# Optimization experiments

Hardware: AMD Instinct MI355X
Metric: run time of the kernel (lower is better)

## Reference

```python
import jax, jax.numpy as jnp
import numpy as np

# Dims: T=out_seq_len, B=batch, D=hidden_dim, H=hidden_dim_de, E=embedding_size, C=feat_channels
T, B, D, H, E, C, FH, FW = 32, 16, 512, 512, 512, 512, 8, 32


def _lstm_dir(x_seq, W_ih, W_hh, b_ih, b_hh, reverse):
    # x_seq: (T, B, D); PyTorch gate order i, f, g, o
    gx = jnp.einsum('tbd,gd->tbg', x_seq, W_ih) + b_ih  # (T, B, 4H)
    Hh = W_hh.shape[1]
    def step(carry, g_t):
        h, c = carry
        g = g_t + h @ W_hh.T + b_hh
        i, f, gg, o = jnp.split(g, 4, axis=-1)
        c = jax.nn.sigmoid(f) * c + jax.nn.sigmoid(i) * jnp.tanh(gg)
        h = jax.nn.sigmoid(o) * jnp.tanh(c)
        return (h, c), h
    init = (jnp.zeros((x_seq.shape[1], Hh), x_seq.dtype),
            jnp.zeros((x_seq.shape[1], Hh), x_seq.dtype))
    _, hs = jax.lax.scan(step, init, gx, reverse=reverse)
    return hs  # (T, B, H)


def setup_inputs() -> dict:
    key = jax.random.key(0)
    ks = jax.random.split(key, 16)
    s = 0.02
    inp = {
        'hidden_en': jax.random.normal(ks[0], (T, B, D), jnp.float32),
        'conv_f': jax.random.normal(ks[1], (B, C, FH, FW), jnp.float32),
        # bidirectional LSTM params (PyTorch layout: W_ih (4H, D), W_hh (4H, H))
        'W_ih_f': jax.random.normal(ks[2], (4 * H, D), jnp.float32) * s,
        'W_hh_f': jax.random.normal(ks[3], (4 * H, H), jnp.float32) * s,
        'b_ih_f': jnp.zeros((4 * H,), jnp.float32),
        'b_hh_f': jnp.zeros((4 * H,), jnp.float32),
        'W_ih_b': jax.random.normal(ks[4], (4 * H, D), jnp.float32) * s,
        'W_hh_b': jax.random.normal(ks[5], (4 * H, H), jnp.float32) * s,
        'b_ih_b': jnp.zeros((4 * H,), jnp.float32),
        'b_hh_b': jnp.zeros((4 * H,), jnp.float32),
        # linear_decode: (H, 2H)
        'W_dec': jax.random.normal(ks[6], (H, 2 * H), jnp.float32) * s,
        'b_dec': jnp.zeros((H,), jnp.float32),
        # conv_em: 3x3, C -> E (OIHW)
        'W_em': jax.random.normal(ks[7], (E, C, 3, 3), jnp.float32) * s,
        'b_em': jnp.zeros((E,), jnp.float32),
        # attention h_em: 1x1 conv == linear H -> E
        'W_hem': jax.random.normal(ks[8], (E, H), jnp.float32) * s,
        'b_hem': jnp.zeros((E,), jnp.float32),
        # conv_att: 1x1 conv E -> 1
        'w_att': jax.random.normal(ks[9], (E,), jnp.float32) * s,
        'b_att': jnp.zeros((), jnp.float32),
    }
    return inp


def reference(hidden_en, conv_f, W_ih_f, W_hh_f, b_ih_f, b_hh_f,
              W_ih_b, W_hh_b, b_ih_b, b_hh_b, W_dec, b_dec,
              W_em, b_em, W_hem, b_hem, w_att, b_att):
    # decoder_ctc: bidirectional LSTM + linear
    h_fwd = _lstm_dir(hidden_en, W_ih_f, W_hh_f, b_ih_f, b_hh_f, reverse=False)
    h_bwd = _lstm_dir(hidden_en, W_ih_b, W_hh_b, b_ih_b, b_hh_b, reverse=True)
    hidden_de = jnp.concatenate([h_fwd, h_bwd], axis=-1) @ W_dec.T + b_dec  # (T, B, H)

    # conv_em: 3x3 same-padding conv, NCHW
    x_em = jax.lax.conv_general_dilated(
        conv_f, W_em, window_strides=(1, 1), padding='SAME',
        dimension_numbers=('NCHW', 'OIHW', 'NCHW')) + b_em[None, :, None, None]  # (B,E,FH,FW)
    att_x_em = jnp.transpose(x_em.reshape(x_em.shape[0], E, -1), (0, 2, 1))  # (B, HW, E)

    # batched attention over all timesteps (dropout is identity at eval)
    h_em = jnp.einsum('tbh,eh->tbe', hidden_de, W_hem) + b_hem  # (T, B, E)
    feat = jnp.tanh(x_em[None] + h_em[:, :, :, None, None])     # (T, B, E, FH, FW)
    scores = jnp.einsum('tbehw,e->tbhw', feat, w_att) + b_att   # (T, B, FH, FW)
    alpha = jax.nn.softmax(scores.reshape(scores.shape[0], scores.shape[1], -1), axis=-1)  # (T,B,HW)
    att = jnp.einsum('tbn,bne->tbe', alpha, att_x_em)           # (T, B, E)

    ctc_out = jnp.concatenate([hidden_de, att], axis=-1)        # (T, B, H+E)
    return jnp.transpose(ctc_out, (1, 0, 2))                    # (B, T, H+E)
```

## Files before the change

### kernel.cpp

```cpp
#include <hip/hip_runtime.h>
#include <hip/hip_bf16.h>
#include <math.h>

#define T_LEN 32
#define BATCH 16
#define DDIM  512
#define HDIM  512
#define EDIM  512
#define CDIM  512
#define FHH   8
#define FWW   32
#define HW    256
#define G4    2048
#define PADH  10
#define PADW  34
#define WLP   520

typedef __attribute__((ext_vector_type(8))) short bf16x8;
typedef __attribute__((ext_vector_type(4))) float f32x4;

__device__ __forceinline__ ushort bfr(float x) {
    union { float f; uint32_t u; } c; c.f = x;
    uint32_t r = (c.u + 0x7FFFu + ((c.u >> 16) & 1u)) >> 16;
    return (ushort)r;
}

__device__ __forceinline__ float frcp(float x) { return __builtin_amdgcn_rcpf(x); }
__device__ __forceinline__ float ftanh(float x) {
    return 1.f - 2.f * frcp(1.f + __expf(2.f * x));
}
__device__ __forceinline__ float fsig(float x) {
    return frcp(1.f + __expf(-x));
}

__device__ __forceinline__ void ld_lds16(const void* g, void* l) {
    __builtin_amdgcn_global_load_lds((const __attribute__((address_space(1))) void*)g,
                                     (__attribute__((address_space(3))) void*)l, 16, 0, 0);
}

__device__ __forceinline__ void st_u16_sc1(ushort* p, ushort v) {
    asm volatile("global_store_short %0, %1, off sc1" :: "v"(p), "v"((uint)v) : "memory");
}
__device__ __forceinline__ void st_i32_sc1(int* p, int v) {
    asm volatile("global_store_dword %0, %1, off sc1" :: "v"(p), "v"(v) : "memory");
}
__device__ __forceinline__ void st_f32_sc1(float* p, float v) {
    asm volatile("global_store_dword %0, %1, off sc1" :: "v"(p), "v"(v) : "memory");
}
__device__ __forceinline__ int ld_i32_sc1(const int* p) {
    int v;
    asm volatile("global_load_dword %0, %1, off sc1\n\ts_waitcnt vmcnt(0)"
                 : "=v"(v) : "v"(p) : "memory");
    return v;
}
__device__ __forceinline__ float ld_f32_sc1(const float* p) {
    float v;
    asm volatile("global_load_dword %0, %1, off sc1\n\ts_waitcnt vmcnt(0)"
                 : "=v"(v) : "v"(p) : "memory");
    return v;
}

struct PrepArgs { const float* s[7]; ushort* d[7]; };
__global__ __launch_bounds__(256) void prep_all(
    PrepArgs a, int* __restrict__ syncbuf,
    const float* __restrict__ conv_f, ushort* __restrict__ padT,
    const float* __restrict__ W_em, ushort* __restrict__ Wt,
    const float* __restrict__ W_dec, ushort* __restrict__ WdecT,
    const float* __restrict__ W_hem, const float* __restrict__ b_dec,
    const float* __restrict__ b_hem, float* __restrict__ b_comb)
{
    __shared__ float tile[32][33];
    const int bid = blockIdx.x, tid = threadIdx.x;
    if (bid < 5120) {
        int i = bid * 256 + tid;
        if (i < 80) st_i32_sc1(syncbuf + i, 0);
        const int e0 = 65536, e1 = 327680, e2 = 589824, e3 = 851968,
                  e4 = 1114112, e5 = 1245184;
        int seg, base;
        if      (i < e0) { seg = 0; base = 0;  }
        else if (i < e1) { seg = 1; base = e0; }
        else if (i < e2) { seg = 2; base = e1; }
        else if (i < e3) { seg = 3; base = e2; }
        else if (i < e4) { seg = 4; base = e3; }
        else if (i < e5) { seg = 5; base = e4; }
        else             { seg = 6; base = e5; }
        int li = i - base;
        float4 v = ((const float4*)a.s[seg])[li];
        ushort4 o;
        o.x = bfr(v.x); o.y = bfr(v.y); o.z = bfr(v.z); o.w = bfr(v.w);
        ((ushort4*)a.d[seg])[li] = o;
        return;
    }
    if (bid < 7168) {
        int id = bid - 5120;
        int s0 = (id & 7) * 32, c0 = ((id >> 3) & 15) * 32, b = id >> 7;
        int lo = tid & 31, hi = tid >> 5;
#pragma unroll
        for (int it = 0; it < 4; ++it) {
            int cl = hi + it * 8;
            tile[cl][lo] = conv_f[((size_t)(b * CDIM + c0 + cl)) * HW + s0 + lo];
        }
        __syncthreads();
#pragma unroll
        for (int it = 0; it < 4; ++it) {
            int sl = hi + it * 8;
            int s = s0 + sl;
            int y = s >> 5, x = s & 31;
            padT[(((size_t)b * PADH + y + 1) * PADW + (x + 1)) * CDIM + c0 + lo] =
                bfr(tile[lo][sl]);
        }
        return;
    }
    if (bid < 7840) {
        int gid = (bid - 7168) * 256 + tid;
        int c4 = gid & 127;
        int cellb = gid >> 7;
        int cell = cellb % 84;
        int b = cellb / 84;
        int y, x;
        if (cell < 34) { y = 0; x = cell; }
        else if (cell < 68) { y = 9; x = cell - 34; }
        else { int k2 = cell - 68; y = 1 + (k2 >> 1); x = (k2 & 1) ? 33 : 0; }
        ((ushort4*)padT)[(((size_t)b * PADH + y) * PADW + x) * (CDIM / 4) + c4] =
            make_ushort4(0, 0, 0, 0);
        return;
    }
    if (bid < 17056) {
        int gid = (bid - 7840) * 256 + tid;
        int c = gid % CDIM;
        int t = gid / CDIM;
        int e = t % EDIM;
        int tap = t / EDIM;
        int dy = tap / 3, dx = tap % 3;
        Wt[gid] = bfr(W_em[((e * CDIM + c) * 3 + dy) * 3 + dx]);
        return;
    }
    if (bid < 17568) {
        int idx = bid - 17056;
        int ht = idx & 15, kt = idx >> 4;
        int h0 = ht * 32, k0 = kt * 32;
        int lo = tid & 31, hi = tid >> 5;
#pragma unroll
        for (int it = 0; it < 4; ++it) {
            int i = hi + it * 8;
            tile[i][lo] = W_dec[(size_t)(h0 + i) * 1024 + k0 + lo];
        }
        __syncthreads();
#pragma unroll
        for (int it = 0; it < 4; ++it) {
            int i = hi + it * 8;
            WdecT[(size_t)(k0 + i) * 512 + h0 + lo] = bfr(tile[lo][i]);
        }
        return;
    }
    {
        int e = (bid - 17568) * 256 + tid;
        float s = b_hem[e];
        const float* wr = W_hem + (size_t)e * 512;
        for (int h = 0; h < 512; ++h) s += wr[h] * b_dec[h];
        b_comb[e] = s;
    }
}

__device__ __forceinline__ void tile64_compute(
    const ushort* Ap0, const ushort* Bp0, int K,
    ushort* smem, int tid, f32x4 (&acc)[2][2])
{
    ushort* As = smem;
    ushort* Bs = smem + 2048;
    const int w = tid >> 6, lane = tid & 63;
    ushort* AsW = &As[w * 512];
    ushort* BsW = &Bs[w * 512];
    const int wm = (w >> 1) * 32, wn = (w & 1) * 32;
    const int kb = (lane >> 4) * 8, fr = lane & 15;
    for (int kk = 0; kk < K; kk += 32) {
        __syncthreads();
        ld_lds16(Ap0 + kk, AsW);
        ld_lds16(Bp0 + kk, BsW);
        __syncthreads();
        bf16x8 af[2], bg[2];
#pragma unroll
        for (int i = 0; i < 2; ++i)
            af[i] = *(const bf16x8*)&As[(wm + i * 16 + fr) * 32 + kb];
#pragma unroll
        for (int j = 0; j < 2; ++j)
            bg[j] = *(const bf16x8*)&Bs[(wn + j * 16 + fr) * 32 + kb];
#pragma unroll
        for (int i = 0; i < 2; ++i)
#pragma unroll
            for (int j = 0; j < 2; ++j)
                acc[i][j] = __builtin_amdgcn_mfma_f32_16x16x32_bf16(af[i], bg[j], acc[i][j], 0, 0, 0);
    }
}

__global__ __launch_bounds__(256) void workers(
    const ushort* __restrict__ padT, const ushort* __restrict__ Wt,
    const float* __restrict__ bias_em, float* __restrict__ xem,
    const ushort* __restrict__ hen_bf,
    const ushort* __restrict__ Wih_f, const ushort* __restrict__ Wih_b,
    const float* __restrict__ b_ih_f, const float* __restrict__ b_hh_f,
    const float* __restrict__ b_ih_b, const float* __restrict__ b_hh_b,
    float* __restrict__ gxT_f, float* __restrict__ gxT_b,
    const ushort* __restrict__ Whem_bf, const ushort* __restrict__ WdecT_bf,
    ushort* __restrict__ Wcomb_bf)
{
    __shared__ ushort smem[4096];
    const int bid = blockIdx.x, tid = threadIdx.x;
    const int w = tid >> 6, lane = tid & 63;
    const int r0 = tid >> 2, c0 = (tid & 3) * 8;
    const int wm = (w >> 1) * 32, wn = (w & 1) * 32;
    const int col = lane & 15, rq = (lane >> 4) * 4;
    f32x4 acc[2][2];
#pragma unroll
    for (int i = 0; i < 2; ++i)
#pragma unroll
        for (int j = 0; j < 2; ++j) acc[i][j] = {0.f, 0.f, 0.f, 0.f};

    if (bid < 512) {
        const int n0 = (bid & 7) * 64, m0 = (bid >> 3) * 64;
        const int b = m0 >> 8, s0 = m0 & 255, y0 = s0 >> 5;
        const int y = y0 + (r0 >> 5), x = r0 & 31;
        const ushort* Abase = padT + (((size_t)b * PADH + y) * PADW + x) * CDIM + c0;
        const ushort* Bbase = Wt + (size_t)(n0 + r0) * CDIM + c0;
        for (int tap = 0; tap < 9; ++tap) {
            const int dy = tap / 3, dx = tap % 3;
            tile64_compute(Abase + ((size_t)dy * PADW + dx) * CDIM,
                           Bbase + (size_t)tap * EDIM * CDIM, 512, smem, tid, acc);
        }
#pragma unroll
        for (int i = 0; i < 2; ++i)
#pragma unroll
            for (int r = 0; r < 4; ++r) {
                int m = m0 + wm + i * 16 + rq + r;
                int s = m & 255;
#pragma unroll
                for (int j2 = 0; j2 < 2; ++j2) {
                    int e = n0 + wn + j2 * 16 + col;
                    xem[((size_t)b * EDIM + e) * HW + s] = acc[i][j2][r] + bias_em[e];
                }
            }
        return;
    }
    if (bid < 1024) {
        const int gi = bid - 512;
        const int dir = gi & 1;
        const int q = gi >> 1;
        const int mt = q >> 5, nt = q & 31;
        const ushort* Bw = dir ? Wih_b : Wih_f;
        const float* bi0 = dir ? b_ih_b : b_ih_f;
        const float* bi1 = dir ? b_hh_b : b_hh_f;
        float* Cg = dir ? gxT_b : gxT_f;
        const int m0 = mt * 64, n0 = nt * 64;
        tile64_compute(hen_bf + (size_t)(m0 + r0) * 512 + c0,
                       Bw + (size_t)(n0 + r0) * 512 + c0, 512, smem, tid, acc);
#pragma unroll
        for (int i = 0; i < 2; ++i)
#pragma unroll
            for (int r = 0; r < 4; ++r) {
                int m = m0 + wm + i * 16 + rq + r;
#pragma unroll
                for (int j2 = 0; j2 < 2; ++j2) {
                    int n = n0 + wn + j2 * 16 + col;
                    Cg[(size_t)m * G4 + (n & 511) * 4 + (n >> 9)] =
                        acc[i][j2][r] + bi0[n] + bi1[n];
                }
            }
        return;
    }
    {
        const int wb = bid - 1024;
        const int mt = wb >> 4, nt = wb & 15;
        const int m0 = mt * 64, n0 = nt * 64;
        tile64_compute(Whem_bf + (size_t)(m0 + r0) * 512 + c0,
                       WdecT_bf + (size_t)(n0 + r0) * 512 + c0, 512, smem, tid, acc);
#pragma unroll
        for (int i = 0; i < 2; ++i)
#pragma unroll
            for (int r = 0; r < 4; ++r) {
                int m = m0 + wm + i * 16 + rq + r;
#pragma unroll
                for (int j2 = 0; j2 < 2; ++j2) {
                    int n = n0 + wn + j2 * 16 + col;
                    Wcomb_bf[(size_t)m * 1024 + n] = bfr(acc[i][j2][r]);
                }
            }
    }
}

__global__ __launch_bounds__(256) void lstm_persist(
    const ushort* __restrict__ Whh_f, const ushort* __restrict__ Whh_b,
    const float* __restrict__ gxT_f, const float* __restrict__ gxT_b,
    ushort* __restrict__ hs_bf, int* __restrict__ flags)
{
    __shared__ ushort smem[64 * WLP];
    const int bid = blockIdx.x, tid = threadIdx.x;
    const int w = tid >> 6, lane = tid & 63;
    const int dir = bid >> 5;
    const int j0 = (bid & 31) * 16;
    const ushort* W = dir ? Whh_b : Whh_f;
    const float* gx = dir ? gxT_b : gxT_f;
#pragma unroll
    for (int i = 0; i < 16; ++i) {
        int row = w * 16 + i;
        int g = row >> 4, jl = row & 15;
        bf16x8 v = *(const bf16x8*)(W + ((size_t)(g * 512 + j0 + jl)) * 512 + lane * 8);
        *(bf16x8*)&smem[row * WLP + lane * 8] = v;
    }
    __syncthreads();
    if (tid >= 64) return;
    __builtin_amdgcn_s_setprio(1);

    const int fr = lane & 15, kq = lane >> 4;
    const int j = j0 + fr;
    const int* fq = &flags[dir * 32 + (lane & 31)];
    f32x4 cr = {0.f, 0.f, 0.f, 0.f};
    for (int step = 0; step < T_LEN; ++step) {
        const int tcur = dir ? (T_LEN - 1 - step) : step;
        float4 gq[4];
#pragma unroll
        for (int r = 0; r < 4; ++r)
            gq[r] = *(const float4*)(gx + (((size_t)tcur * BATCH + kq * 4 + r) * 512 + j) * 4);
        f32x4 acc[4];
#pragma unroll
        for (int g = 0; g < 4; ++g) acc[g] = {0.f, 0.f, 0.f, 0.f};
        if (step > 0) {
            const int tprev = dir ? tcur + 1 : tcur - 1;
            const ushort* hp = hs_bf + ((size_t)tprev * BATCH + fr) * 1024 + dir * 512 + kq * 8;
            bf16x8 hreg[16];
#pragma unroll
            for (int u = 0; u < 16; ++u)
                asm volatile("global_load_dwordx4 %0, %1, off sc1"
                             : "=v"(hreg[u]) : "v"(hp + u * 32));
            asm volatile("s_waitcnt vmcnt(0)" ::: "memory");
            __builtin_amdgcn_sched_barrier(0);
#pragma unroll
            for (int u = 0; u < 16; ++u) {
#pragma unroll
                for (int g = 0; g < 4; ++g) {
                    bf16x8 bb = *(const bf16x8*)&smem[(g * 16 + fr) * WLP + kq * 8 + u * 32];
                    acc[g] = __builtin_amdgcn_mfma_f32_16x16x32_bf16(hreg[u], bb, acc[g], 0, 0, 0);
                }
            }
        }
#pragma unroll
        for (int r = 0; r < 4; ++r) {
            int b = kq * 4 + r;
            float gi = gq[r].x + acc[0][r];
            float gf = gq[r].y + acc[1][r];
            float gg = gq[r].z + acc[2][r];
            float go = gq[r].w + acc[3][r];
            float si = fsig(gi), sf = fsig(gf), so = fsig(go);
            float c = sf * cr[r] + si * ftanh(gg);
            cr[r] = c;
            float h = so * ftanh(c);
            st_u16_sc1(hs_bf + ((size_t)tcur * BATCH + b) * 1024 + dir * 512 + j, bfr(h));
        }
        if (step < T_LEN - 1) {
            asm volatile("s_waitcnt vmcnt(0)" ::: "memory");
            if (lane == 0) st_i32_sc1(&flags[bid], step + 1);
            const int need = step + 1;
            for (;;) {
                int v = ld_i32_sc1(fq);
                if (__all(v >= need)) break;
                __builtin_amdgcn_s_sleep(1);
            }
        }
    }
}

__global__ __launch_bounds__(256) void tail(
    const ushort* __restrict__ hs_bf, const ushort* __restrict__ Wdec_bf,
    const float* __restrict__ b_dec, float* __restrict__ out,
    const ushort* __restrict__ Wcomb_bf, const float* __restrict__ b_comb,
    float* __restrict__ h_em,
    const float* __restrict__ xem, const float* __restrict__ watt,
    int* __restrict__ syncbuf)
{
    __shared__ ushort smem[4096];
    int* hcnt = syncbuf + 64;
    const int bid = blockIdx.x, tid = threadIdx.x;
    const int w = tid >> 6, lane = tid & 63;
    const int r0 = tid >> 2, c0 = (tid & 3) * 8;
    const int wm = (w >> 1) * 32, wn = (w & 1) * 32;
    const int col = lane & 15, rq = (lane >> 4) * 4;

    if (bid < 128) {
        f32x4 acc[2][2];
#pragma unroll
        for (int i = 0; i < 2; ++i)
#pragma unroll
            for (int j = 0; j < 2; ++j) acc[i][j] = {0.f, 0.f, 0.f, 0.f};
        if (bid < 64) {
            const int mt = bid >> 3, nt = bid & 7;
            const int m0 = mt * 64, n0 = nt * 64;
            tile64_compute(hs_bf + (size_t)(m0 + r0) * 1024 + c0,
                           Wdec_bf + (size_t)(n0 + r0) * 1024 + c0, 1024, smem, tid, acc);
#pragma unroll
            for (int i = 0; i < 2; ++i)
#pragma unroll
                for (int r = 0; r < 4; ++r) {
                    int m = m0 + wm + i * 16 + rq + r;
                    int t = m >> 4, b = m & 15;
#pragma unroll
                    for (int j2 = 0; j2 < 2; ++j2) {
                        int n = n0 + wn + j2 * 16 + col;
                        out[((size_t)(b * T_LEN + t)) * 1024 + n] = acc[i][j2][r] + b_dec[n];
                    }
                }
        } else {
            const int blk = bid - 64;
            const int mt = blk >> 3, nt = blk & 7;
            const int m0 = mt * 64, n0 = nt * 64;
            tile64_compute(hs_bf + (size_t)(m0 + r0) * 1024 + c0,
                           Wcomb_bf + (size_t)(n0 + r0) * 1024 + c0, 1024, smem, tid, acc);
#pragma unroll
            for (int i = 0; i < 2; ++i)
#pragma unroll
                for (int r = 0; r < 4; ++r) {
                    int m = m0 + wm + i * 16 + rq + r;
#pragma unroll
                    for (int j2 = 0; j2 < 2; ++j2) {
                        int n = n0 + wn + j2 * 16 + col;
                        st_f32_sc1(&h_em[(size_t)m * 512 + n], acc[i][j2][r] + b_comb[n]);
                    }
                }
            asm volatile("s_waitcnt vmcnt(0)" ::: "memory");
            __syncthreads();
            if (tid == 0) atomicAdd(&hcnt[mt], 1);
        }
        return;
    }

    {
        int i = bid - 128;
        int k = i >> 3;
        int b = ((i & 7) << 1) | (k & 1);
        int t = k >> 1;
        int tb = t * 16 + b;
        const int mt = tb >> 6;
        if (tid == 0) {
            while (ld_i32_sc1(&hcnt[mt]) < 8) __builtin_amdgcn_s_sleep(8);
        }
        __syncthreads();
        float* fs = (float*)smem;
        float* hl = fs;
        float* wl = fs + 512;
        float* al = fs + 1024;
        float* red = fs + 1280;
        for (int q = tid; q < 512; q += 256) {
            hl[q] = ld_f32_sc1(&h_em[(size_t)tb * 512 + q]);
            wl[q] = watt[q];
        }
        __syncthreads();
        const float* xb = xem + (size_t)b * EDIM * HW;
        float sc = 0.f;
#pragma unroll 4
        for (int e = 0; e < 512; ++e)
            sc += ftanh(xb[(size_t)e * HW + tid] + hl[e]) * wl[e];
        float m = sc;
#pragma unroll
        for (int o = 32; o; o >>= 1) m = fmaxf(m, __shfl_xor(m, o));
        if ((tid & 63) == 0) red[tid >> 6] = m;
        __syncthreads();
        m = fmaxf(fmaxf(red[0], red[1]), fmaxf(red[2], red[3]));
        float ex = __expf(sc - m);
        float s = ex;
#pragma unroll
        for (int o = 32; o; o >>= 1) s += __shfl_xor(s, o);
        if ((tid & 63) == 0) red[4 + (tid >> 6)] = s;
        __syncthreads();
        s = red[4] + red[5] + red[6] + red[7];
        al[tid] = ex * frcp(s);
        __syncthreads();
        float* ob = out + ((size_t)(b * T_LEN + t)) * 1024 + 512;
        for (int eo = 0; eo < 512; eo += 256) {
            int e = eo + tid;
            const float* xr = xb + (size_t)e * HW;
            float acc2 = 0.f;
#pragma unroll 4
            for (int n = 0; n < 256; n += 4) {
                float4 v = *(const float4*)&xr[n];
                acc2 += al[n] * v.x + al[n + 1] * v.y + al[n + 2] * v.z + al[n + 3] * v.w;
            }
            ob[e] = acc2;
        }
    }
}

extern "C" void kernel_launch(void* const* d_in, const int* in_sizes, int n_in,
                              void* d_out, int out_size, void* d_ws, size_t ws_size,
                              hipStream_t stream) {
    const float* hidden_en = (const float*)d_in[0];
    const float* conv_f    = (const float*)d_in[1];
    const float* W_ih_f    = (const float*)d_in[2];
    const float* W_hh_f    = (const float*)d_in[3];
    const float* b_ih_f    = (const float*)d_in[4];
    const float* b_hh_f    = (const float*)d_in[5];
    const float* W_ih_b    = (const float*)d_in[6];
    const float* W_hh_b    = (const float*)d_in[7];
    const float* b_ih_b    = (const float*)d_in[8];
    const float* b_hh_b    = (const float*)d_in[9];
    const float* W_dec     = (const float*)d_in[10];
    const float* b_dec     = (const float*)d_in[11];
    const float* W_em      = (const float*)d_in[12];
    const float* b_em      = (const float*)d_in[13];
    const float* W_hem     = (const float*)d_in[14];
    const float* b_hem     = (const float*)d_in[15];
    const float* w_att     = (const float*)d_in[16];
    float* out = (float*)d_out;

    char* p = (char*)d_ws;
    auto alloc = [&](size_t bytes) { void* r = p; p += (bytes + 255) & ~(size_t)255; return r; };
    float*    gxT_f   = (float*)alloc((size_t)T_LEN * BATCH * G4 * 4);
    float*    gxT_b   = (float*)alloc((size_t)T_LEN * BATCH * G4 * 4);
    float*    h_em    = (float*)alloc((size_t)T_LEN * BATCH * 512 * 4);
    float*    x_em    = (float*)alloc((size_t)BATCH * EDIM * HW * 4);
    ushort*   padT    = (ushort*)alloc((size_t)BATCH * PADH * PADW * CDIM * 2);
    ushort*   Wt      = (ushort*)alloc((size_t)9 * EDIM * CDIM * 2);
    ushort*   hen_bf  = (ushort*)alloc((size_t)T_LEN * BATCH * DDIM * 2);
    ushort*   Wihf_bf = (ushort*)alloc((size_t)G4 * DDIM * 2);
    ushort*   Wihb_bf = (ushort*)alloc((size_t)G4 * DDIM * 2);
    ushort*   Whhf_bf = (ushort*)alloc((size_t)G4 * HDIM * 2);
    ushort*   Whhb_bf = (ushort*)alloc((size_t)G4 * HDIM * 2);
    ushort*   Wdec_bf = (ushort*)alloc((size_t)HDIM * 1024 * 2);
    ushort*   Whem_bf = (ushort*)alloc((size_t)EDIM * HDIM * 2);
    ushort*   WdecT_bf= (ushort*)alloc((size_t)1024 * 512 * 2);
    ushort*   Wcomb_bf= (ushort*)alloc((size_t)512 * 1024 * 2);
    float*    b_comb  = (float*)alloc(512 * 4);
    ushort*   hs_bf   = (ushort*)alloc((size_t)T_LEN * BATCH * 1024 * 2);
    int*      syncbuf = (int*)alloc(512);

    PrepArgs pa;
    pa.s[0] = hidden_en; pa.d[0] = hen_bf;
    pa.s[1] = W_ih_f;    pa.d[1] = Wihf_bf;
    pa.s[2] = W_ih_b;    pa.d[2] = Wihb_bf;
    pa.s[3] = W_hh_f;    pa.d[3] = Whhf_bf;
    pa.s[4] = W_hh_b;    pa.d[4] = Whhb_bf;
    pa.s[5] = W_dec;     pa.d[5] = Wdec_bf;
    pa.s[6] = W_hem;     pa.d[6] = Whem_bf;
    prep_all<<<17570, 256, 0, stream>>>(pa, syncbuf, conv_f, padT, W_em, Wt,
                                        W_dec, WdecT_bf, W_hem, b_dec, b_hem, b_comb);

    workers<<<1152, 256, 0, stream>>>(padT, Wt, b_em, x_em, hen_bf,
                                      Wihf_bf, Wihb_bf, b_ih_f, b_hh_f,
                                      b_ih_b, b_hh_b, gxT_f, gxT_b,
                                      Whem_bf, WdecT_bf, Wcomb_bf);

    lstm_persist<<<64, 256, 0, stream>>>(Whhf_bf, Whhb_bf, gxT_f, gxT_b,
                                         hs_bf, syncbuf);

    tail<<<640, 256, 0, stream>>>(hs_bf, Wdec_bf, b_dec, out,
                                  Wcomb_bf, b_comb, h_em, x_em, w_att, syncbuf);
}
```

Baseline: 287.4 us.

## Fuse LSTM recurrence into worker kernel with per-timestep-tile readiness counters

The persistent LSTM recurrence now runs as the first 64 blocks of a merged kernel that also holds the input-projection GEMM, the conv GEMM and the weight-combine GEMM. Input-projection tiles are ordered by timestep, with the backward direction reversed, and each completed tile bumps a counter so the recurrence can start as soon as the timesteps it needs are ready. This is meant to overlap the serial recurrence with the conv and other GEMM work instead of running them back to back. The gate-preactivation load for the next step is also prefetched asynchronously, and the flag poll reads four flags per vector load. The risk is that the 64 recurrence blocks, each using about 96KB of LDS, must be resident alongside the spin-waiting producers, and conv blocks may compete with the recurrence for compute.

After: 280.2 us. -2.5%, faster.

```diff
diff --git a/kernel.cpp b/kernel.cpp
--- a/kernel.cpp
+++ b/kernel.cpp
@@ -18,6 +18,7 @@
 
 typedef __attribute__((ext_vector_type(8))) short bf16x8;
 typedef __attribute__((ext_vector_type(4))) float f32x4;
+typedef __attribute__((ext_vector_type(4))) int i32x4;
 
 __device__ __forceinline__ ushort bfr(float x) {
     union { float f; uint32_t u; } c; c.f = x;
@@ -53,10 +54,21 @@
                  : "=v"(v) : "v"(p) : "memory");
     return v;
 }
+__device__ __forceinline__ i32x4 ld_i32x4_sc1(const int* p) {
+    i32x4 v;
+    asm volatile("global_load_dwordx4 %0, %1, off sc1\n\ts_waitcnt vmcnt(0)"
+                 : "=v"(v) : "v"(p) : "memory");
+    return v;
+}
 __device__ __forceinline__ float ld_f32_sc1(const float* p) {
     float v;
     asm volatile("global_load_dword %0, %1, off sc1\n\ts_waitcnt vmcnt(0)"
                  : "=v"(v) : "v"(p) : "memory");
+    return v;
+}
+__device__ __forceinline__ f32x4 ld_f32x4_sc1_async(const float* p) {
+    f32x4 v;
+    asm volatile("global_load_dwordx4 %0, %1, off sc1" : "=v"(v) : "v"(p));
     return v;
 }
 
@@ -73,7 +85,7 @@
     const int bid = blockIdx.x, tid = threadIdx.x;
     if (bid < 5120) {
         int i = bid * 256 + tid;
-        if (i < 80) st_i32_sc1(syncbuf + i, 0);
+        if (i < 128) st_i32_sc1(syncbuf + i, 0);
         const int e0 = 65536, e1 = 327680, e2 = 589824, e3 = 851968,
                   e4 = 1114112, e5 = 1245184;
         int seg, base;
@@ -193,20 +205,123 @@
     }
 }
 
-__global__ __launch_bounds__(256) void workers(
-    const ushort* __restrict__ padT, const ushort* __restrict__ Wt,
-    const float* __restrict__ bias_em, float* __restrict__ xem,
+__global__ __launch_bounds__(256) void fused_main(
+    const ushort* __restrict__ Whh_f, const ushort* __restrict__ Whh_b,
+    float* __restrict__ gxT_f, float* __restrict__ gxT_b,
     const ushort* __restrict__ hen_bf,
     const ushort* __restrict__ Wih_f, const ushort* __restrict__ Wih_b,
     const float* __restrict__ b_ih_f, const float* __restrict__ b_hh_f,
     const float* __restrict__ b_ih_b, const float* __restrict__ b_hh_b,
-    float* __restrict__ gxT_f, float* __restrict__ gxT_b,
+    ushort* __restrict__ hs_bf,
+    int* __restrict__ syncbuf,
+    const ushort* __restrict__ padT, const ushort* __restrict__ Wt,
+    const float* __restrict__ bias_em, float* __restrict__ xem,
     const ushort* __restrict__ Whem_bf, const ushort* __restrict__ WdecT_bf,
     ushort* __restrict__ Wcomb_bf)
 {
-    __shared__ ushort smem[4096];
+    __shared__ ushort smem[49152];
     const int bid = blockIdx.x, tid = threadIdx.x;
     const int w = tid >> 6, lane = tid & 63;
+    int* flags = syncbuf;
+    int* gcnt  = syncbuf + 64;
+
+    if (bid < 64) {
+        const int dir = bid >> 5;
+        const int j0 = (bid & 31) * 16;
+        const ushort* W = dir ? Whh_b : Whh_f;
+        const float* gx = dir ? gxT_b : gxT_f;
+#pragma unroll
+        for (int i = 0; i < 16; ++i) {
+            int row = w * 16 + i;
+            int g = row >> 4, jl = row & 15;
+            bf16x8 v = *(const bf16x8*)(W + ((size_t)(g * 512 + j0 + jl)) * 512 + lane * 8);
+            *(bf16x8*)&smem[row * WLP + lane * 8] = v;
+        }
+        __syncthreads();
+        if (tid >= 64) return;
+        __builtin_amdgcn_s_setprio(1);
+
+        const int fr = lane & 15, kq = lane >> 4;
+        const int j = j0 + fr;
+        const int* fq4 = &flags[dir * 32 + (lane & 7) * 4];
+        const int t0 = dir ? (T_LEN - 1) : 0;
+        int mt_ok = t0 >> 2;
+        {
+            const int* gp = &gcnt[dir * 8 + mt_ok];
+            while (ld_i32_sc1(gp) < 32) __builtin_amdgcn_s_sleep(4);
+        }
+        f32x4 gq[4];
+#pragma unroll
+        for (int r = 0; r < 4; ++r)
+            gq[r] = ld_f32x4_sc1_async(gx + (((size_t)t0 * BATCH + kq * 4 + r) * 512 + j) * 4);
+        f32x4 cr = {0.f, 0.f, 0.f, 0.f};
+        for (int step = 0; step < T_LEN; ++step) {
+            const int tcur = dir ? (T_LEN - 1 - step) : step;
+            if (step > 0) {
+                const int need = step;
+                for (;;) {
+                    i32x4 v = ld_i32x4_sc1(fq4);
+                    int mn = min(min(v[0], v[1]), min(v[2], v[3]));
+                    if (__all(mn >= need)) break;
+                    __builtin_amdgcn_s_sleep(1);
+                }
+            }
+            f32x4 acc[4];
+#pragma unroll
+            for (int g = 0; g < 4; ++g) acc[g] = {0.f, 0.f, 0.f, 0.f};
+            if (step > 0) {
+                const int tprev = dir ? tcur + 1 : tcur - 1;
+                const ushort* hp = hs_bf + ((size_t)tprev * BATCH + fr) * 1024 + dir * 512 + kq * 8;
+                bf16x8 hreg[16];
+#pragma unroll
+                for (int u = 0; u < 16; ++u)
+                    asm volatile("global_load_dwordx4 %0, %1, off sc1"
+                                 : "=v"(hreg[u]) : "v"(hp + u * 32));
+                asm volatile("s_waitcnt vmcnt(0)" ::: "memory");
+                __builtin_amdgcn_sched_barrier(0);
+#pragma unroll
+                for (int u = 0; u < 16; ++u) {
+#pragma unroll
+                    for (int g = 0; g < 4; ++g) {
+                        bf16x8 bb = *(const bf16x8*)&smem[(g * 16 + fr) * WLP + kq * 8 + u * 32];
+                        acc[g] = __builtin_amdgcn_mfma_f32_16x16x32_bf16(hreg[u], bb, acc[g], 0, 0, 0);
+                    }
+                }
+            } else {
+                asm volatile("s_waitcnt vmcnt(0)" ::: "memory");
+                __builtin_amdgcn_sched_barrier(0);
+            }
+#pragma unroll
+            for (int r = 0; r < 4; ++r) {
+                int b = kq * 4 + r;
+                float gi = gq[r][0] + acc[0][r];
+                float gf = gq[r][1] + acc[1][r];
+                float gg = gq[r][2] + acc[2][r];
+                float go = gq[r][3] + acc[3][r];
+                float si = fsig(gi), sf = fsig(gf), so = fsig(go);
+                float c = sf * cr[r] + si * ftanh(gg);
+                cr[r] = c;
+                float h = so * ftanh(c);
+                st_u16_sc1(hs_bf + ((size_t)tcur * BATCH + b) * 1024 + dir * 512 + j, bfr(h));
+            }
+            if (step < T_LEN - 1) {
+                asm volatile("s_waitcnt vmcnt(0)" ::: "memory");
+                if (lane == 0) st_i32_sc1(&flags[bid], step + 1);
+                const int tnext = dir ? tcur - 1 : tcur + 1;
+                const int mtn = tnext >> 2;
+                if (mtn != mt_ok) {
+                    const int* gp = &gcnt[dir * 8 + mtn];
+                    while (ld_i32_sc1(gp) < 32) __builtin_amdgcn_s_sleep(2);
+                    mt_ok = mtn;
+                }
+#pragma unroll
+                for (int r = 0; r < 4; ++r)
+                    gq[r] = ld_f32x4_sc1_async(gx + (((size_t)tnext * BATCH + kq * 4 + r) * 512 + j) * 4);
+            }
+        }
+        return;
+    }
+
     const int r0 = tid >> 2, c0 = (tid & 3) * 8;
     const int wm = (w >> 1) * 32, wn = (w & 1) * 32;
     const int col = lane & 15, rq = (lane >> 4) * 4;
@@ -216,8 +331,40 @@
 #pragma unroll
         for (int j = 0; j < 2; ++j) acc[i][j] = {0.f, 0.f, 0.f, 0.f};
 
-    if (bid < 512) {
-        const int n0 = (bid & 7) * 64, m0 = (bid >> 3) * 64;
+    if (bid < 576) {
+        const int gi = bid - 64;
+        const int dir = gi & 1;
+        const int q = gi >> 1;
+        const int nt = q & 31;
+        const int mt0 = q >> 5;
+        const int mtile = dir ? (7 - mt0) : mt0;
+        const ushort* Bw = dir ? Wih_b : Wih_f;
+        const float* bi0 = dir ? b_ih_b : b_ih_f;
+        const float* bi1 = dir ? b_hh_b : b_hh_f;
+        float* Cg = dir ? gxT_b : gxT_f;
+        const int m0 = mtile * 64, n0 = nt * 64;
+        tile64_compute(hen_bf + (size_t)(m0 + r0) * 512 + c0,
+                       Bw + (size_t)(n0 + r0) * 512 + c0, 512, smem, tid, acc);
+#pragma unroll
+        for (int i = 0; i < 2; ++i)
+#pragma unroll
+            for (int r = 0; r < 4; ++r) {
+                int m = m0 + wm + i * 16 + rq + r;
+#pragma unroll
+                for (int j2 = 0; j2 < 2; ++j2) {
+                    int n = n0 + wn + j2 * 16 + col;
+                    st_f32_sc1(&Cg[(size_t)m * G4 + (n & 511) * 4 + (n >> 9)],
+                               acc[i][j2][r] + bi0[n] + bi1[n]);
+                }
+            }
+        asm volatile("s_waitcnt vmcnt(0)" ::: "memory");
+        __syncthreads();
+        if (tid == 0) atomicAdd(&gcnt[dir * 8 + mtile], 1);
+        return;
+    }
+    if (bid < 1088) {
+        const int cbid = bid - 576;
+        const int n0 = (cbid & 7) * 64, m0 = (cbid >> 3) * 64;
         const int b = m0 >> 8, s0 = m0 & 255, y0 = s0 >> 5;
         const int y = y0 + (r0 >> 5), x = r0 & 31;
         const ushort* Abase = padT + (((size_t)b * PADH + y) * PADW + x) * CDIM + c0;
@@ -241,34 +388,8 @@
             }
         return;
     }
-    if (bid < 1024) {
-        const int gi = bid - 512;
-        const int dir = gi & 1;
-        const int q = gi >> 1;
-        const int mt = q >> 5, nt = q & 31;
-        const ushort* Bw = dir ? Wih_b : Wih_f;
-        const float* bi0 = dir ? b_ih_b : b_ih_f;
-        const float* bi1 = dir ? b_hh_b : b_hh_f;
-        float* Cg = dir ? gxT_b : gxT_f;
-        const int m0 = mt * 64, n0 = nt * 64;
-        tile64_compute(hen_bf + (size_t)(m0 + r0) * 512 + c0,
-                       Bw + (size_t)(n0 + r0) * 512 + c0, 512, smem, tid, acc);
-#pragma unroll
-        for (int i = 0; i < 2; ++i)
-#pragma unroll
-            for (int r = 0; r < 4; ++r) {
-                int m = m0 + wm + i * 16 + rq + r;
-#pragma unroll
-                for (int j2 = 0; j2 < 2; ++j2) {
-                    int n = n0 + wn + j2 * 16 + col;
-                    Cg[(size_t)m * G4 + (n & 511) * 4 + (n >> 9)] =
-                        acc[i][j2][r] + bi0[n] + bi1[n];
-                }
-            }
-        return;
-    }
     {
-        const int wb = bid - 1024;
+        const int wb = bid - 1088;
         const int mt = wb >> 4, nt = wb & 15;
         const int m0 = mt * 64, n0 = nt * 64;
         tile64_compute(Whem_bf + (size_t)(m0 + r0) * 512 + c0,
@@ -284,87 +405,6 @@
                     Wcomb_bf[(size_t)m * 1024 + n] = bfr(acc[i][j2][r]);
                 }
             }
-    }
-}
-
-__global__ __launch_bounds__(256) void lstm_persist(
-    const ushort* __restrict__ Whh_f, const ushort* __restrict__ Whh_b,
-    const float* __restrict__ gxT_f, const float* __restrict__ gxT_b,
-    ushort* __restrict__ hs_bf, int* __restrict__ flags)
-{
-    __shared__ ushort smem[64 * WLP];
-    const int bid = blockIdx.x, tid = threadIdx.x;
-    const int w = tid >> 6, lane = tid & 63;
-    const int dir = bid >> 5;
-    const int j0 = (bid & 31) * 16;
-    const ushort* W = dir ? Whh_b : Whh_f;
-    const float* gx = dir ? gxT_b : gxT_f;
-#pragma unroll
-    for (int i = 0; i < 16; ++i) {
-        int row = w * 16 + i;
-        int g = row >> 4, jl = row & 15;
-        bf16x8 v = *(const bf16x8*)(W + ((size_t)(g * 512 + j0 + jl)) * 512 + lane * 8);
-        *(bf16x8*)&smem[row * WLP + lane * 8] = v;
-    }
-    __syncthreads();
-    if (tid >= 64) return;
-    __builtin_amdgcn_s_setprio(1);
-
-    const int fr = lane & 15, kq = lane >> 4;
-    const int j = j0 + fr;
-    const int* fq = &flags[dir * 32 + (lane & 31)];
-    f32x4 cr = {0.f, 0.f, 0.f, 0.f};
-    for (int step = 0; step < T_LEN; ++step) {
-        const int tcur = dir ? (T_LEN - 1 - step) : step;
-        float4 gq[4];
-#pragma unroll
-        for (int r = 0; r < 4; ++r)
-            gq[r] = *(const float4*)(gx + (((size_t)tcur * BATCH + kq * 4 + r) * 512 + j) * 4);
-        f32x4 acc[4];
-#pragma unroll
-        for (int g = 0; g < 4; ++g) acc[g] = {0.f, 0.f, 0.f, 0.f};
-        if (step > 0) {
-            const int tprev = dir ? tcur + 1 : tcur - 1;
-            const ushort* hp = hs_bf + ((size_t)tprev * BATCH + fr) * 1024 + dir * 512 + kq * 8;
-            bf16x8 hreg[16];
-#pragma unroll
-            for (int u = 0; u < 16; ++u)
-                asm volatile("global_load_dwordx4 %0, %1, off sc1"
-                             : "=v"(hreg[u]) : "v"(hp + u * 32));
-            asm volatile("s_waitcnt vmcnt(0)" ::: "memory");
-            __builtin_amdgcn_sched_barrier(0);
-#pragma unroll
-            for (int u = 0; u < 16; ++u) {
-#pragma unroll
-                for (int g = 0; g < 4; ++g) {
-                    bf16x8 bb = *(const bf16x8*)&smem[(g * 16 + fr) * WLP + kq * 8 + u * 32];
-                    acc[g] = __builtin_amdgcn_mfma_f32_16x16x32_bf16(hreg[u], bb, acc[g], 0, 0, 0);
-                }
-            }
-        }
-#pragma unroll
-        for (int r = 0; r < 4; ++r) {
-            int b = kq * 4 + r;
-            float gi = gq[r].x + acc[0][r];
-            float gf = gq[r].y + acc[1][r];
-            float gg = gq[r].z + acc[2][r];
-            float go = gq[r].w + acc[3][r];
-            float si = fsig(gi), sf = fsig(gf), so = fsig(go);
-            float c = sf * cr[r] + si * ftanh(gg);
-            cr[r] = c;
-            float h = so * ftanh(c);
-            st_u16_sc1(hs_bf + ((size_t)tcur * BATCH + b) * 1024 + dir * 512 + j, bfr(h));
-        }
-        if (step < T_LEN - 1) {
-            asm volatile("s_waitcnt vmcnt(0)" ::: "memory");
-            if (lane == 0) st_i32_sc1(&flags[bid], step + 1);
-            const int need = step + 1;
-            for (;;) {
-                int v = ld_i32_sc1(fq);
-                if (__all(v >= need)) break;
-                __builtin_amdgcn_s_sleep(1);
-            }
-        }
     }
 }
 
@@ -377,7 +417,7 @@
     int* __restrict__ syncbuf)
 {
     __shared__ ushort smem[4096];
-    int* hcnt = syncbuf + 64;
+    int* hcnt = syncbuf + 96;
     const int bid = blockIdx.x, tid = threadIdx.x;
     const int w = tid >> 6, lane = tid & 63;
     const int r0 = tid >> 2, c0 = (tid & 3) * 8;
@@ -528,7 +568,7 @@
     ushort*   Wcomb_bf= (ushort*)alloc((size_t)512 * 1024 * 2);
     float*    b_comb  = (float*)alloc(512 * 4);
     ushort*   hs_bf   = (ushort*)alloc((size_t)T_LEN * BATCH * 1024 * 2);
-    int*      syncbuf = (int*)alloc(512);
+    int*      syncbuf = (int*)alloc(1024);
 
     PrepArgs pa;
     pa.s[0] = hidden_en; pa.d[0] = hen_bf;
@@ -541,13 +581,11 @@
     prep_all<<<17570, 256, 0, stream>>>(pa, syncbuf, conv_f, padT, W_em, Wt,
                                         W_dec, WdecT_bf, W_hem, b_dec, b_hem, b_comb);
 
-    workers<<<1152, 256, 0, stream>>>(padT, Wt, b_em, x_em, hen_bf,
-                                      Wihf_bf, Wihb_bf, b_ih_f, b_hh_f,
-                                      b_ih_b, b_hh_b, gxT_f, gxT_b,
-                                      Whem_bf, WdecT_bf, Wcomb_bf);
-
-    lstm_persist<<<64, 256, 0, stream>>>(Whhf_bf, Whhb_bf, gxT_f, gxT_b,
-                                         hs_bf, syncbuf);
+    fused_main<<<1216, 256, 0, stream>>>(Whhf_bf, Whhb_bf, gxT_f, gxT_b, hen_bf,
+                                         Wihf_bf, Wihb_bf, b_ih_f, b_hh_f,
+                                         b_ih_b, b_hh_b, hs_bf, syncbuf,
+                                         padT, Wt, b_em, x_em,
+                                         Whem_bf, WdecT_bf, Wcomb_bf);
 
     tail<<<640, 256, 0, stream>>>(hs_bf, Wdec_bf, b_dec, out,
                                   Wcomb_bf, b_comb, h_em, x_em, w_att, syncbuf);
```
